# Kernel tuning notes

Measured on AMD Instinct MI355X. Metric: run time of the kernel, lower is better.

## Reference

```python
import jax, jax.numpy as jnp
import numpy as np
import math

B, T, Z, H, DOF = 256, 200, 64, 256, 12
NUM_LINKS = 13
POS_DIM = (NUM_LINKS + 1) * 3  # 42
TIME_BANDS = 6
TIME_DIM = 2 * TIME_BANDS + 1  # 13
ACTION_SCALE = 0.25
TRACK_ALPHA = 1.0
SIGMA_MIN, SIGMA_MAX = 0.05, 0.5


def setup_inputs() -> dict:
    key = jax.random.key(0)
    ks = iter(jax.random.split(key, 32))
    rn = lambda shape, s=0.1: jax.random.normal(next(ks), shape, jnp.float32) * s
    inp = {
        'z': jax.random.normal(next(ks), (B, Z), jnp.float32),
        'W_hz': rn((H, Z)), 'b_hz': rn((H,)),
        'W_cz': rn((H, Z)), 'b_cz': rn((H,)),
        'Wih': rn((4 * H, DOF + Z + TIME_DIM)), 'Whh': rn((4 * H, H)),
        'bih': rn((4 * H,)), 'bhh': rn((4 * H,)),
        'Wp1': rn((H, H)), 'bp1': rn((H,)),
        'Wp2': rn((DOF, H)), 'bp2': rn((DOF,)),
        'Wo1': rn((H, H)), 'bo1': rn((H,)),
        'Wo2': rn((3, H)), 'bo2': rn((3,)),
        'Wv': rn((POS_DIM, H)), 'bv': rn((POS_DIM,)),
        'Wfk': rn((NUM_LINKS * 3, DOF)), 'bfk': rn((NUM_LINKS * 3,)),
        'pos_mean': jax.random.normal(next(ks), (NUM_LINKS + 1, 3), jnp.float32),
        'pos_std': 0.5 + jax.random.uniform(next(ks), (NUM_LINKS + 1, 3), jnp.float32),
        'joint_lower': -jnp.ones((DOF,), jnp.float32),
        'joint_upper': jnp.ones((DOF,), jnp.float32),
        'default_dof_pos': jnp.zeros((DOF,), jnp.float32),
    }
    return inp


def _time_features():
    t = jnp.linspace(0.0, 1.0, T)
    feats = [t]
    for k in range(TIME_BANDS):
        f = 2.0 ** k
        feats.append(jnp.sin(2 * math.pi * f * t))
        feats.append(jnp.cos(2 * math.pi * f * t))
    return jnp.stack(feats, axis=-1)  # [T, TIME_DIM]


def reference(z, W_hz, b_hz, W_cz, b_cz, Wih, Whh, bih, bhh,
              Wp1, bp1, Wp2, bp2, Wo1, bo1, Wo2, bo2, Wv, bv, Wfk, bfk,
              pos_mean, pos_std, joint_lower, joint_upper, default_dof_pos):
    joint_range = (joint_upper - joint_lower) / 2.0
    joint_mean = (joint_upper + joint_lower) / 2.0
    time_feats = _time_features()  # [T, TIME_DIM]

    h0 = z @ W_hz.T + b_hz  # [B,H]
    c0 = z @ W_cz.T + b_cz
    prev0 = jnp.broadcast_to(default_dof_pos, (B, DOF))

    def step(carry, tf):
        h, c, prev = carry
        prev_norm = (prev - joint_mean) / joint_range
        x = jnp.concatenate([prev_norm, z, jnp.broadcast_to(tf, (B, TIME_DIM))], axis=-1)
        g = x @ Wih.T + bih + h @ Whh.T + bhh  # [B,4H]
        i, f, gg, o = jnp.split(g, 4, axis=-1)
        c_new = jax.nn.sigmoid(f) * c + jax.nn.sigmoid(i) * jnp.tanh(gg)
        h_new = jax.nn.sigmoid(o) * jnp.tanh(c_new)
        action = jnp.tanh(jax.nn.relu(h_new @ Wp1.T + bp1) @ Wp2.T + bp2)
        target = action * ACTION_SCALE + default_dof_pos
        cur = prev + TRACK_ALPHA * (target - prev)
        clamped = jnp.clip(cur, joint_lower, joint_upper)
        cur_in = cur + jax.lax.stop_gradient(clamped - cur)  # straight-through clamp
        obj = jax.nn.relu(h_new @ Wo1.T + bo1) @ Wo2.T + bo2
        return (h_new, c_new, jax.lax.stop_gradient(cur_in)), (h_new, action, cur, obj)

    _, (H_seq, actions, joints, objs) = jax.lax.scan(step, (h0, c0, prev0), time_feats)
    # [T,B,*] -> [B,T,*]
    H_seq = jnp.swapaxes(H_seq, 0, 1)
    actions_seq = jnp.swapaxes(actions, 0, 1)
    joint_traj = jnp.swapaxes(joints, 0, 1)
    object_traj = jnp.swapaxes(objs, 0, 1)

    agent_traj = joint_traj @ Wfk.T + bfk  # FK: [B,T,39]
    combined = jnp.concatenate([agent_traj, object_traj], axis=-1)  # [B,T,42]
    combined_rs = combined.reshape(B, T, NUM_LINKS + 1, 3)
    graph_x_mu = ((combined_rs - pos_mean) / pos_std).reshape(B, T, POS_DIM)

    sigma = SIGMA_MIN + (SIGMA_MAX - SIGMA_MIN) * jax.nn.sigmoid(H_seq @ Wv.T + bv)
    log_sigma_pos = jnp.log(sigma)
    return (graph_x_mu, joint_traj, actions_seq, log_sigma_pos)
```

## Files before the change

kernel.cpp:

```cpp
#include <hip/hip_runtime.h>
#include <math.h>

#define B_ 256
#define T_ 200
#define H_ 256
#define DOF_ 12

typedef __bf16 bf16;
typedef __bf16 bf16x8 __attribute__((ext_vector_type(8)));
typedef float f32x4 __attribute__((ext_vector_type(4)));
typedef unsigned long long u64;

#define XK 288
#define XPAD 296
#define P1PAD 264

#define PI_D 3.14159265358979323846

#define OFF_TF     0u
#define OFF_TCONP  10400u
#define OFF_ZCP    829600u
#define OFF_H0     1878176u
#define OFF_C0     2140320u
#define OFF_WCOMB  2402464u
#define OFF_WP1    2992288u
#define OFF_WP2    3123360u
#define OFF_WO1    3131552u
#define OFF_WO2    3262624u
#define OFF_WV     3270816u
#define OFF_HX     3295392u
#define OFF_HSEQ   3819680u

__device__ __forceinline__ float sigf(float x) { return 1.f / (1.f + __expf(-x)); }
__device__ __forceinline__ float tanh_f(float x) {
  float a = fabsf(x);
  float e = __expf(-2.f * a);
  float t = (1.f - e) * __builtin_amdgcn_rcpf(1.f + e);
  return x < 0.f ? -t : t;
}

#define LBAR() asm volatile("s_waitcnt lgkmcnt(0)\n\ts_barrier" ::: "memory")

__global__ void k_tfeat(float* tf) {
  int i = blockIdx.x * blockDim.x + threadIdx.x;
  if (i >= T_ * 13) return;
  int t = i / 13, j = i % 13;
  float tv = (float)t / 199.f;
  float v;
  if (j == 0) v = tv;
  else {
    int k = (j - 1) >> 1;
    float f = (float)(1 << k);
    double arg = 2.0 * PI_D * (double)f * (double)tv;
    v = (j & 1) ? (float)sin(arg) : (float)cos(arg);
  }
  tf[i] = v;
}

__global__ void k_prep(const float* __restrict__ tf, const float* __restrict__ Wih,
                       const float* __restrict__ z,
                       const float* __restrict__ bih, const float* __restrict__ bhh,
                       const float* __restrict__ Whz, const float* __restrict__ bhz,
                       const float* __restrict__ Wcz, const float* __restrict__ bcz,
                       float* tconp, float* zcp, float* h0, float* c0) {
  int i = blockIdx.x * blockDim.x + threadIdx.x;
  if (i < 204800) {
    int g = i & 3, u = (i >> 2) & 255, t = i >> 10;
    int n = g * 256 + u;
    float s = 0.f;
    #pragma unroll
    for (int j = 0; j < 13; ++j) s += tf[t * 13 + j] * Wih[n * 89 + 76 + j];
    tconp[i] = s;
    return;
  }
  i -= 204800;
  if (i < 262144) {
    int r = i & 3, g = (i >> 2) & 3, tid = (i >> 4) & 255, bid = i >> 12;
    int quarter = bid >> 4, grp = bid & 15;
    int wv = tid >> 6, ln = tid & 63, lr = ln & 15, lq = (ln >> 4) & 3;
    int b = grp * 16 + lq * 4 + r;
    int n = g * 256 + 64 * quarter + 16 * wv + lr;
    float s = bih[n] + bhh[n];
    for (int k = 0; k < 64; ++k) s += z[b * 64 + k] * Wih[n * 89 + 12 + k];
    zcp[i] = s;
    return;
  }
  i -= 262144;
  if (i < 65536) {
    int b = i / 256, u = i % 256;
    float s = bhz[u];
    for (int k = 0; k < 64; ++k) s += z[b * 64 + k] * Whz[u * 64 + k];
    h0[i] = s;
    return;
  }
  i -= 65536;
  if (i < 65536) {
    int b = i / 256, u = i % 256;
    float s = bcz[u];
    for (int k = 0; k < 64; ++k) s += z[b * 64 + k] * Wcz[u * 64 + k];
    c0[i] = s;
  }
}

__global__ void k_cast(const float* __restrict__ Whh, const float* __restrict__ Wih,
                       const float* __restrict__ Wp1, const float* __restrict__ Wp2,
                       const float* __restrict__ Wo1, const float* __restrict__ Wo2,
                       const float* __restrict__ Wv,
                       bf16* Wcomb, bf16* Wp1b, bf16* Wp2b, bf16* Wo1b,
                       bf16* Wo2b, bf16* Wvb) {
  int i = blockIdx.x * blockDim.x + threadIdx.x;
  if (i < 294912) {
    int n = i / XK, k = i % XK;
    float v = (k < 256) ? Whh[n * 256 + k]
            : ((k < 268) ? Wih[n * 89 + (k - 256)] : 0.f);
    Wcomb[i] = (bf16)v;
    return;
  }
  i -= 294912;
  if (i < 65536) { Wp1b[i] = (bf16)Wp1[i]; return; }
  i -= 65536;
  if (i < 4096) { int r = i / 256; Wp2b[i] = (bf16)((r < 12) ? Wp2[i] : 0.f); return; }
  i -= 4096;
  if (i < 65536) { Wo1b[i] = (bf16)Wo1[i]; return; }
  i -= 65536;
  if (i < 4096) { int r = i / 256; Wo2b[i] = (bf16)((r < 3) ? Wo2[i] : 0.f); return; }
  i -= 4096;
  if (i < 12288) { int r = i / 256; Wvb[i] = (bf16)((r < 42) ? Wv[i] : 0.f); }
}

__global__ __launch_bounds__(256, 1) void k_recur(
    const float* __restrict__ zcp, const float* __restrict__ tconp,
    const float* __restrict__ h0, const float* __restrict__ c0,
    const bf16* __restrict__ Wcomb, const bf16* __restrict__ Wp1b,
    const bf16* __restrict__ Wp2b,
    const float* __restrict__ bp1, const float* __restrict__ bp2,
    const float* __restrict__ jlo, const float* __restrict__ jhi,
    const float* __restrict__ ddp,
    u64* hxt,
    bf16* __restrict__ Hseq, float* __restrict__ outJ, float* __restrict__ outA) {
  __shared__ bf16 xbuf[16][XPAD];
  __shared__ bf16 w1[272][P1PAD];
  __shared__ bf16 p1buf[16][P1PAD];
  const int tid = threadIdx.x;
  const int wv = tid >> 6, ln = tid & 63, lr = ln & 15, lq = ln >> 4;
  const int bid = blockIdx.x;
  const int quarter = bid >> 4, grp = bid & 15;
  const int b0 = grp * 16;
  const int u_gl = 64 * quarter + 16 * wv + lr;

  for (int i = tid; i < 272 * 32; i += 256) {
    int r = i >> 5, c8 = (i & 31) * 8;
    bf16x8 v = (r < 256)
      ? *reinterpret_cast<const bf16x8*>(&Wp1b[r * 256 + c8])
      : *reinterpret_cast<const bf16x8*>(&Wp2b[(r - 256) * 256 + c8]);
    *reinterpret_cast<bf16x8*>(&w1[r][c8]) = v;
  }
  for (int i = tid; i < 16 * XPAD; i += 256) {
    int r = i / XPAD, c = i % XPAD;
    float v = 0.f;
    if (c < 256) v = h0[(b0 + r) * 256 + c];
    else if (c < 268) {
      int d = c - 256;
      float lo = jlo[d], hi = jhi[d];
      v = (ddp[d] - 0.5f * (hi + lo)) / (0.5f * (hi - lo));
    }
    xbuf[r][c] = (bf16)v;
  }

  f32x4 wc[4][9];
  #pragma unroll
  for (int g = 0; g < 4; ++g)
    #pragma unroll
    for (int kt = 0; kt < 9; ++kt)
      wc[g][kt] = *reinterpret_cast<const f32x4*>(
          &Wcomb[(size_t)(g * 256 + u_gl) * XK + kt * 32 + lq * 8]);
  #pragma unroll
  for (int kt = 0; kt < 9; ++kt)
    asm volatile("" : "+a"(wc[0][kt]), "+a"(wc[1][kt]),
                      "+a"(wc[2][kt]), "+a"(wc[3][kt]));

  float c_reg[4];
  #pragma unroll
  for (int r = 0; r < 4; ++r) c_reg[r] = c0[(b0 + lq * 4 + r) * 256 + u_gl];
  const int zc_i = (bid * 256 + tid) * 16;
  int tc_i = u_gl * 4;
  int hs_i = ((b0 + lq * 4) * T_) * 256 + u_gl;
  const int pw_i = (grp * 8 + quarter) * 512 + (16 * wv + lr) * 8 + lq * 2;
  const int ru = tid >> 2, rlq = tid & 3;
  const int rrow0 = rlq * 4;
  const int q1 = (quarter + 1) & 3, q2 = (quarter + 2) & 3, q3 = (quarter + 3) & 3;
  const int pr1 = (grp * 8 + q1) * 512 + ru * 8 + rlq * 2;
  const int pr2 = (grp * 8 + q2) * 512 + ru * 8 + rlq * 2;
  const int pr3 = (grp * 8 + q3) * 512 + ru * 8 + rlq * 2;

  float bp1r[4];
  #pragma unroll
  for (int jn = 0; jn < 4; ++jn) bp1r[jn] = bp1[64 * wv + 16 * jn + lr];
  float bp2r = 0.f, ddr = 0.f, lor = -1.f, hir = 1.f;
  if (lr < 12) { bp2r = bp2[lr]; ddr = ddp[lr]; lor = jlo[lr]; hir = jhi[lr]; }
  const float jmr = 0.5f * (hir + lor), jrr = 0.5f * (hir - lor);

  __syncthreads();
  bool dead = false;

  for (int t = 0; t < T_; ++t) {
    f32x4 zc[4], tcv;
    #pragma unroll
    for (int g = 0; g < 4; ++g)
      zc[g] = *reinterpret_cast<const f32x4*>(zcp + zc_i + g * 4);
    tcv = *reinterpret_cast<const f32x4*>(tconp + tc_i);
    tc_i += 1024;

    f32x4 ac[4];
    #pragma unroll
    for (int g = 0; g < 4; ++g) ac[g] = (f32x4){0.f, 0.f, 0.f, 0.f};
    #pragma unroll
    for (int kt = 0; kt < 9; ++kt) {
      bf16x8 a = *reinterpret_cast<const bf16x8*>(&xbuf[lr][kt * 32 + lq * 8]);
      asm volatile("" : "+a"(wc[0][kt]), "+a"(wc[1][kt]),
                        "+a"(wc[2][kt]), "+a"(wc[3][kt]));
      #pragma unroll
      for (int g = 0; g < 4; ++g)
        ac[g] = __builtin_amdgcn_mfma_f32_16x16x32_bf16(
            a, __builtin_bit_cast(bf16x8, wc[g][kt]), ac[g], 0, 0, 0);
    }
    #pragma unroll
    for (int g = 0; g < 4; ++g) ac[g] += zc[g] + tcv[g];
    LBAR();

    const unsigned int want = t + 1;
    bf16 hb[4];
    unsigned short s4[4];
    #pragma unroll
    for (int r = 0; r < 4; ++r) {
      float cn = sigf(ac[1][r]) * c_reg[r] + sigf(ac[0][r]) * tanh_f(ac[2][r]);
      float hn = sigf(ac[3][r]) * tanh_f(cn);
      c_reg[r] = cn;
      bf16 h = (bf16)hn;
      hb[r] = h;
      s4[r] = __builtin_bit_cast(unsigned short, h);
    }
    {
      u64 q0 = ((u64)want << 32) | (u64)s4[0] | ((u64)s4[1] << 16);
      u64 qq1 = ((u64)want << 32) | (u64)s4[2] | ((u64)s4[3] << 16);
      int pwi = pw_i + (t & 1) * 2048;
      __hip_atomic_store(hxt + pwi, q0, __ATOMIC_RELAXED, __HIP_MEMORY_SCOPE_AGENT);
      __hip_atomic_store(hxt + pwi + 1, qq1, __ATOMIC_RELAXED, __HIP_MEMORY_SCOPE_AGENT);
    }
    #pragma unroll
    for (int r = 0; r < 4; ++r) {
      xbuf[lq * 4 + r][u_gl] = hb[r];
      Hseq[hs_i + r * (T_ * 256)] = hb[r];
    }
    hs_i += 256;

    u64 pa0, pa1, pb0, pb1, pc0, pc1;
    {
      const int so = (t & 1) * 2048;
      int guard = 1 << 16;
      for (;;) {
        pa0 = __hip_atomic_load(hxt + pr1 + so, __ATOMIC_RELAXED, __HIP_MEMORY_SCOPE_AGENT);
        pa1 = __hip_atomic_load(hxt + pr1 + so + 1, __ATOMIC_RELAXED, __HIP_MEMORY_SCOPE_AGENT);
        pb0 = __hip_atomic_load(hxt + pr2 + so, __ATOMIC_RELAXED, __HIP_MEMORY_SCOPE_AGENT);
        pb1 = __hip_atomic_load(hxt + pr2 + so + 1, __ATOMIC_RELAXED, __HIP_MEMORY_SCOPE_AGENT);
        pc0 = __hip_atomic_load(hxt + pr3 + so, __ATOMIC_RELAXED, __HIP_MEMORY_SCOPE_AGENT);
        pc1 = __hip_atomic_load(hxt + pr3 + so + 1, __ATOMIC_RELAXED, __HIP_MEMORY_SCOPE_AGENT);
        int ok = ((unsigned)(pa0 >> 32) == want) & ((unsigned)(pa1 >> 32) == want) &
                 ((unsigned)(pb0 >> 32) == want) & ((unsigned)(pb1 >> 32) == want) &
                 ((unsigned)(pc0 >> 32) == want) & ((unsigned)(pc1 >> 32) == want);
        if (__all(ok)) break;
        if (dead || --guard == 0) { dead = true; break; }
      }
    }
    {
      int col1 = 64 * q1 + ru, col2 = 64 * q2 + ru, col3 = 64 * q3 + ru;
      xbuf[rrow0 + 0][col1] = __builtin_bit_cast(bf16, (unsigned short)(pa0));
      xbuf[rrow0 + 1][col1] = __builtin_bit_cast(bf16, (unsigned short)(pa0 >> 16));
      xbuf[rrow0 + 2][col1] = __builtin_bit_cast(bf16, (unsigned short)(pa1));
      xbuf[rrow0 + 3][col1] = __builtin_bit_cast(bf16, (unsigned short)(pa1 >> 16));
      xbuf[rrow0 + 0][col2] = __builtin_bit_cast(bf16, (unsigned short)(pb0));
      xbuf[rrow0 + 1][col2] = __builtin_bit_cast(bf16, (unsigned short)(pb0 >> 16));
      xbuf[rrow0 + 2][col2] = __builtin_bit_cast(bf16, (unsigned short)(pb1));
      xbuf[rrow0 + 3][col2] = __builtin_bit_cast(bf16, (unsigned short)(pb1 >> 16));
      xbuf[rrow0 + 0][col3] = __builtin_bit_cast(bf16, (unsigned short)(pc0));
      xbuf[rrow0 + 1][col3] = __builtin_bit_cast(bf16, (unsigned short)(pc0 >> 16));
      xbuf[rrow0 + 2][col3] = __builtin_bit_cast(bf16, (unsigned short)(pc1));
      xbuf[rrow0 + 3][col3] = __builtin_bit_cast(bf16, (unsigned short)(pc1 >> 16));
    }
    LBAR();

    {
      f32x4 pa[4];
      #pragma unroll
      for (int jn = 0; jn < 4; ++jn)
        pa[jn] = (f32x4){bp1r[jn], bp1r[jn], bp1r[jn], bp1r[jn]};
      #pragma unroll
      for (int kt = 0; kt < 8; ++kt) {
        bf16x8 av = *reinterpret_cast<const bf16x8*>(&xbuf[lr][kt * 32 + lq * 8]);
        #pragma unroll
        for (int jn = 0; jn < 4; ++jn) {
          bf16x8 bv = *reinterpret_cast<const bf16x8*>(
              &w1[64 * wv + 16 * jn + lr][kt * 32 + lq * 8]);
          pa[jn] = __builtin_amdgcn_mfma_f32_16x16x32_bf16(av, bv, pa[jn], 0, 0, 0);
        }
      }
      #pragma unroll
      for (int jn = 0; jn < 4; ++jn)
        #pragma unroll
        for (int r = 0; r < 4; ++r)
          p1buf[lq * 4 + r][64 * wv + 16 * jn + lr] = (bf16)fmaxf(pa[jn][r], 0.f);
    }
    LBAR();

    if (wv == 0) {
      f32x4 acc = {0.f, 0.f, 0.f, 0.f};
      #pragma unroll
      for (int kt = 0; kt < 8; ++kt) {
        bf16x8 ap = *reinterpret_cast<const bf16x8*>(&p1buf[lr][kt * 32 + lq * 8]);
        bf16x8 w2 = *reinterpret_cast<const bf16x8*>(&w1[256 + lr][kt * 32 + lq * 8]);
        acc = __builtin_amdgcn_mfma_f32_16x16x32_bf16(ap, w2, acc, 0, 0, 0);
      }
      if (lr < 12) {
        #pragma unroll
        for (int r = 0; r < 4; ++r) {
          int b = lq * 4 + r;
          float act = tanh_f(acc[r] + bp2r);
          float curp = act * 0.25f + ddr;
          float cl = fminf(fmaxf(curp, lor), hir);
          if (quarter == 0) {
            size_t o = ((size_t)(b0 + b) * T_ + t) * 12 + lr;
            outA[o] = act;
            outJ[o] = curp;
          }
          xbuf[b][256 + lr] = (bf16)((cl - jmr) / jrr);
        }
      }
    }
    LBAR();
  }
}

__global__ __launch_bounds__(256) void k_post(
    const bf16* __restrict__ Hseq, const bf16* __restrict__ Wo1b,
    const bf16* __restrict__ Wo2b, const bf16* __restrict__ Wvb,
    const float* __restrict__ bo1, const float* __restrict__ bo2,
    const float* __restrict__ bv,
    const float* __restrict__ Wfk, const float* __restrict__ bfk,
    const float* __restrict__ pm, const float* __restrict__ ps,
    const float* __restrict__ joints, float* __restrict__ out0,
    float* __restrict__ out3) {
  __shared__ bf16 u1buf[16][P1PAD];
  __shared__ float objbuf[16][3];
  __shared__ float jbuf[16][12];
  const int tid = threadIdx.x;
  const int wv = tid >> 6;
  const int ln = tid & 63;
  const int lr = ln & 15;
  const int lq = ln >> 4;

  bf16x8 wo1f[4][8];
  float bo1r[4];
  #pragma unroll
  for (int jn = 0; jn < 4; ++jn) {
    int n0 = wv * 64 + jn * 16;
    bo1r[jn] = bo1[n0 + lr];
    #pragma unroll
    for (int kt = 0; kt < 8; ++kt)
      wo1f[jn][kt] = *reinterpret_cast<const bf16x8*>(
          &Wo1b[(size_t)(n0 + lr) * 256 + kt * 32 + lq * 8]);
  }
  const int col = (wv - 1) * 16 + lr;
  bf16x8 wvf[8];
  float bvr = 0.f;
  if (wv >= 1) {
    #pragma unroll
    for (int kt = 0; kt < 8; ++kt)
      wvf[kt] = *reinterpret_cast<const bf16x8*>(
          &Wvb[(size_t)col * 256 + kt * 32 + lq * 8]);
    bvr = (col < 42) ? bv[col] : 0.f;
  }
  bf16x8 wo2f[8];
  if (wv == 0) {
    #pragma unroll
    for (int kt = 0; kt < 8; ++kt)
      wo2f[kt] = *reinterpret_cast<const bf16x8*>(
          &Wo2b[(size_t)lr * 256 + kt * 32 + lq * 8]);
  }

  for (int it = 0; it < 10; ++it) {
    int tt = blockIdx.x * 10 + it;
    size_t r0 = (size_t)tt * 16;
    bf16x8 ah[8];
    #pragma unroll
    for (int kt = 0; kt < 8; ++kt)
      ah[kt] = *reinterpret_cast<const bf16x8*>(&Hseq[(r0 + lr) * 256 + kt * 32 + lq * 8]);
    #pragma unroll
    for (int jn = 0; jn < 4; ++jn) {
      int n0 = wv * 64 + jn * 16;
      float bb = bo1r[jn];
      f32x4 acc = {bb, bb, bb, bb};
      #pragma unroll
      for (int kt = 0; kt < 8; ++kt)
        acc = __builtin_amdgcn_mfma_f32_16x16x32_bf16(ah[kt], wo1f[jn][kt], acc, 0, 0, 0);
      #pragma unroll
      for (int r = 0; r < 4; ++r)
        u1buf[lq * 4 + r][n0 + lr] = (bf16)fmaxf(acc[r], 0.f);
    }
    if (wv >= 1) {
      f32x4 acc = {bvr, bvr, bvr, bvr};
      #pragma unroll
      for (int kt = 0; kt < 8; ++kt)
        acc = __builtin_amdgcn_mfma_f32_16x16x32_bf16(ah[kt], wvf[kt], acc, 0, 0, 0);
      if (col < 42) {
        #pragma unroll
        for (int r = 0; r < 4; ++r) {
          float s = 0.05f + 0.45f * sigf(acc[r]);
          out3[(r0 + lq * 4 + r) * 42 + col] = __logf(s);
        }
      }
    }
    if (tid < 192) {
      int rr = tid / 12, d = tid % 12;
      jbuf[rr][d] = joints[(r0 + rr) * 12 + d];
    }
    __syncthreads();
    if (wv == 0) {
      bf16x8 ap[8];
      #pragma unroll
      for (int kt = 0; kt < 8; ++kt)
        ap[kt] = *reinterpret_cast<const bf16x8*>(&u1buf[lr][kt * 32 + lq * 8]);
      f32x4 acc = {0.f, 0.f, 0.f, 0.f};
      #pragma unroll
      for (int kt = 0; kt < 8; ++kt)
        acc = __builtin_amdgcn_mfma_f32_16x16x32_bf16(ap[kt], wo2f[kt], acc, 0, 0, 0);
      if (lr < 3) {
        #pragma unroll
        for (int r = 0; r < 4; ++r)
          objbuf[lq * 4 + r][lr] = acc[r] + bo2[lr];
      }
    }
    __syncthreads();
    for (int e = tid; e < 16 * 42; e += 256) {
      int rr = e / 42, pd = e % 42;
      float v;
      if (pd < 39) {
        float s = bfk[pd];
        #pragma unroll
        for (int d = 0; d < 12; ++d) s += jbuf[rr][d] * Wfk[pd * 12 + d];
        v = s;
      } else v = objbuf[rr][pd - 39];
      out0[(r0 + rr) * 42 + pd] = (v - pm[pd]) / ps[pd];
    }
    __syncthreads();
  }
}

extern "C" void kernel_launch(void* const* d_in, const int* in_sizes, int n_in,
                              void* d_out, int out_size, void* d_ws, size_t ws_size,
                              hipStream_t stream) {
  const float* z   = (const float*)d_in[0];
  const float* Whz = (const float*)d_in[1];
  const float* bhz = (const float*)d_in[2];
  const float* Wcz = (const float*)d_in[3];
  const float* bcz = (const float*)d_in[4];
  const float* Wih = (const float*)d_in[5];
  const float* Whh = (const float*)d_in[6];
  const float* bih = (const float*)d_in[7];
  const float* bhh = (const float*)d_in[8];
  const float* Wp1 = (const float*)d_in[9];
  const float* bp1 = (const float*)d_in[10];
  const float* Wp2 = (const float*)d_in[11];
  const float* bp2 = (const float*)d_in[12];
  const float* Wo1 = (const float*)d_in[13];
  const float* bo1 = (const float*)d_in[14];
  const float* Wo2 = (const float*)d_in[15];
  const float* bo2 = (const float*)d_in[16];
  const float* Wv  = (const float*)d_in[17];
  const float* bv  = (const float*)d_in[18];
  const float* Wfk = (const float*)d_in[19];
  const float* bfk = (const float*)d_in[20];
  const float* pm  = (const float*)d_in[21];
  const float* ps  = (const float*)d_in[22];
  const float* jlo = (const float*)d_in[23];
  const float* jhi = (const float*)d_in[24];
  const float* ddp = (const float*)d_in[25];

  char* ws = (char*)d_ws;
  float* tf    = (float*)(ws + OFF_TF);
  float* tconp = (float*)(ws + OFF_TCONP);
  float* zcp   = (float*)(ws + OFF_ZCP);
  float* h0    = (float*)(ws + OFF_H0);
  float* c0    = (float*)(ws + OFF_C0);
  bf16* Wcomb  = (bf16*)(ws + OFF_WCOMB);
  bf16* Wp1b   = (bf16*)(ws + OFF_WP1);
  bf16* Wp2b   = (bf16*)(ws + OFF_WP2);
  bf16* Wo1b   = (bf16*)(ws + OFF_WO1);
  bf16* Wo2b   = (bf16*)(ws + OFF_WO2);
  bf16* Wvb    = (bf16*)(ws + OFF_WV);
  u64* hxt     = (u64*)(ws + OFF_HX);
  bf16* Hseq   = (bf16*)(ws + OFF_HSEQ);

  float* out  = (float*)d_out;
  float* out0 = out;
  float* outJ = out + 2150400;
  float* outA = out + 2764800;
  float* out3 = out + 3379200;

  k_tfeat<<<11, 256, 0, stream>>>(tf);
  k_prep<<<2336, 256, 0, stream>>>(tf, Wih, z, bih, bhh, Whz, bhz, Wcz, bcz,
                                   tconp, zcp, h0, c0);
  k_cast<<<1744, 256, 0, stream>>>(Whh, Wih, Wp1, Wp2, Wo1, Wo2, Wv,
                                   Wcomb, Wp1b, Wp2b, Wo1b, Wo2b, Wvb);
  k_recur<<<64, 256, 0, stream>>>(zcp, tconp, h0, c0, Wcomb, Wp1b, Wp2b,
                                  bp1, bp2, jlo, jhi, ddp, hxt,
                                  Hseq, outJ, outA);
  k_post<<<320, 256, 0, stream>>>(Hseq, Wo1b, Wo2b, Wvb, bo1, bo2, bv,
                                  Wfk, bfk, pm, ps, outJ, out0, out3);
}
```

Measured before the change: 965.7 us.

## Process two batch groups per block to overlap cross-block polling with compute

Each recurrent block now handles two 16-row batch groups, A and B, halving the grid from 64 to 32 blocks. After computing both groups' LSTM gates, the block polls for group A's remote hidden state and runs A's policy heads while B's neighbour data is still arriving, hiding part of the inter-block wait. The Wp1 weights move from shared memory into AGPR registers, freeing LDS for the second x buffer. The cost is more register pressure and twice the serial work per block each step.

```diff
diff --git a/kernel.cpp b/kernel.cpp
--- a/kernel.cpp
+++ b/kernel.cpp
@@ -138,33 +138,41 @@
     const float* __restrict__ ddp,
     u64* hxt,
     bf16* __restrict__ Hseq, float* __restrict__ outJ, float* __restrict__ outA) {
-  __shared__ bf16 xbuf[16][XPAD];
-  __shared__ bf16 w1[272][P1PAD];
+  __shared__ bf16 xbufA[16][XPAD];
+  __shared__ bf16 xbufB[16][XPAD];
   __shared__ bf16 p1buf[16][P1PAD];
+  __shared__ bf16 w2[16][P1PAD];
   const int tid = threadIdx.x;
   const int wv = tid >> 6, ln = tid & 63, lr = ln & 15, lq = ln >> 4;
   const int bid = blockIdx.x;
-  const int quarter = bid >> 4, grp = bid & 15;
-  const int b0 = grp * 16;
+  const int quarter = bid >> 3, j = bid & 7;
+  const int gA = 2 * j, gB = 2 * j + 1;
+  const int b0A = gA * 16, b0B = gB * 16;
   const int u_gl = 64 * quarter + 16 * wv + lr;
 
-  for (int i = tid; i < 272 * 32; i += 256) {
+  for (int i = tid; i < 16 * 32; i += 256) {
     int r = i >> 5, c8 = (i & 31) * 8;
-    bf16x8 v = (r < 256)
-      ? *reinterpret_cast<const bf16x8*>(&Wp1b[r * 256 + c8])
-      : *reinterpret_cast<const bf16x8*>(&Wp2b[(r - 256) * 256 + c8]);
-    *reinterpret_cast<bf16x8*>(&w1[r][c8]) = v;
+    *reinterpret_cast<bf16x8*>(&w2[r][c8]) =
+        *reinterpret_cast<const bf16x8*>(&Wp2b[r * 256 + c8]);
   }
   for (int i = tid; i < 16 * XPAD; i += 256) {
     int r = i / XPAD, c = i % XPAD;
-    float v = 0.f;
-    if (c < 256) v = h0[(b0 + r) * 256 + c];
-    else if (c < 268) {
+    float vA = 0.f;
+    if (c < 256) vA = 0.f;
+    if (c < 256) {
+      xbufA[r][c] = (bf16)h0[(b0A + r) * 256 + c];
+      xbufB[r][c] = (bf16)h0[(b0B + r) * 256 + c];
+    } else if (c < 268) {
       int d = c - 256;
       float lo = jlo[d], hi = jhi[d];
-      v = (ddp[d] - 0.5f * (hi + lo)) / (0.5f * (hi - lo));
+      bf16 pv = (bf16)((ddp[d] - 0.5f * (hi + lo)) / (0.5f * (hi - lo)));
+      xbufA[r][c] = pv;
+      xbufB[r][c] = pv;
+    } else {
+      xbufA[r][c] = (bf16)0.f;
+      xbufB[r][c] = (bf16)0.f;
     }
-    xbuf[r][c] = (bf16)v;
+    (void)vA;
   }
 
   f32x4 wc[4][9];
@@ -174,24 +182,45 @@
     for (int kt = 0; kt < 9; ++kt)
       wc[g][kt] = *reinterpret_cast<const f32x4*>(
           &Wcomb[(size_t)(g * 256 + u_gl) * XK + kt * 32 + lq * 8]);
+  f32x4 wp[4][8];
+  #pragma unroll
+  for (int jn = 0; jn < 4; ++jn)
+    #pragma unroll
+    for (int kt = 0; kt < 8; ++kt)
+      wp[jn][kt] = *reinterpret_cast<const f32x4*>(
+          &Wp1b[(size_t)(64 * wv + 16 * jn + lr) * 256 + kt * 32 + lq * 8]);
   #pragma unroll
   for (int kt = 0; kt < 9; ++kt)
     asm volatile("" : "+a"(wc[0][kt]), "+a"(wc[1][kt]),
                       "+a"(wc[2][kt]), "+a"(wc[3][kt]));
-
-  float c_reg[4];
-  #pragma unroll
-  for (int r = 0; r < 4; ++r) c_reg[r] = c0[(b0 + lq * 4 + r) * 256 + u_gl];
-  const int zc_i = (bid * 256 + tid) * 16;
+  #pragma unroll
+  for (int kt = 0; kt < 8; ++kt)
+    asm volatile("" : "+a"(wp[0][kt]), "+a"(wp[1][kt]),
+                      "+a"(wp[2][kt]), "+a"(wp[3][kt]));
+
+  float cA[4], cB[4];
+  #pragma unroll
+  for (int r = 0; r < 4; ++r) {
+    cA[r] = c0[(b0A + lq * 4 + r) * 256 + u_gl];
+    cB[r] = c0[(b0B + lq * 4 + r) * 256 + u_gl];
+  }
+  const int zc_iA = ((quarter * 16 + gA) * 256 + tid) * 16;
+  const int zc_iB = ((quarter * 16 + gB) * 256 + tid) * 16;
   int tc_i = u_gl * 4;
-  int hs_i = ((b0 + lq * 4) * T_) * 256 + u_gl;
-  const int pw_i = (grp * 8 + quarter) * 512 + (16 * wv + lr) * 8 + lq * 2;
+  int hs_iA = ((b0A + lq * 4) * T_) * 256 + u_gl;
+  int hs_iB = ((b0B + lq * 4) * T_) * 256 + u_gl;
+  const int pwA = (gA * 8 + quarter) * 512 + (16 * wv + lr) * 8 + lq * 2;
+  const int pwB = (gB * 8 + quarter) * 512 + (16 * wv + lr) * 8 + lq * 2;
   const int ru = tid >> 2, rlq = tid & 3;
   const int rrow0 = rlq * 4;
   const int q1 = (quarter + 1) & 3, q2 = (quarter + 2) & 3, q3 = (quarter + 3) & 3;
-  const int pr1 = (grp * 8 + q1) * 512 + ru * 8 + rlq * 2;
-  const int pr2 = (grp * 8 + q2) * 512 + ru * 8 + rlq * 2;
-  const int pr3 = (grp * 8 + q3) * 512 + ru * 8 + rlq * 2;
+  const int prA1 = (gA * 8 + q1) * 512 + ru * 8 + rlq * 2;
+  const int prA2 = (gA * 8 + q2) * 512 + ru * 8 + rlq * 2;
+  const int prA3 = (gA * 8 + q3) * 512 + ru * 8 + rlq * 2;
+  const int prB1 = (gB * 8 + q1) * 512 + ru * 8 + rlq * 2;
+  const int prB2 = (gB * 8 + q2) * 512 + ru * 8 + rlq * 2;
+  const int prB3 = (gB * 8 + q3) * 512 + ru * 8 + rlq * 2;
+  const int col1 = 64 * q1 + ru, col2 = 64 * q2 + ru, col3 = 64 * q3 + ru;
 
   float bp1r[4];
   #pragma unroll
@@ -203,141 +232,144 @@
   __syncthreads();
   bool dead = false;
 
+#define GATES(XB, ZCI, CREG, PWI, HSI)                                         \
+  {                                                                            \
+    f32x4 zc_[4], tcv_;                                                        \
+    _Pragma("unroll") for (int g = 0; g < 4; ++g)                              \
+        zc_[g] = *reinterpret_cast<const f32x4*>(zcp + (ZCI) + g * 4);         \
+    tcv_ = *reinterpret_cast<const f32x4*>(tconp + tc_i);                      \
+    f32x4 ac_[4];                                                              \
+    _Pragma("unroll") for (int g = 0; g < 4; ++g)                              \
+        ac_[g] = (f32x4){0.f, 0.f, 0.f, 0.f};                                  \
+    _Pragma("unroll") for (int kt = 0; kt < 9; ++kt) {                         \
+      bf16x8 a_ = *reinterpret_cast<const bf16x8*>(&XB[lr][kt * 32 + lq * 8]); \
+      _Pragma("unroll") for (int g = 0; g < 4; ++g)                            \
+          ac_[g] = __builtin_amdgcn_mfma_f32_16x16x32_bf16(                    \
+              a_, __builtin_bit_cast(bf16x8, wc[g][kt]), ac_[g], 0, 0, 0);     \
+    }                                                                          \
+    _Pragma("unroll") for (int g = 0; g < 4; ++g) ac_[g] += zc_[g] + tcv_[g];  \
+    LBAR();                                                                    \
+    unsigned short s4_[4];                                                     \
+    bf16 hb_[4];                                                               \
+    _Pragma("unroll") for (int r = 0; r < 4; ++r) {                            \
+      float cn_ = sigf(ac_[1][r]) * CREG[r] + sigf(ac_[0][r]) * tanh_f(ac_[2][r]); \
+      float hn_ = sigf(ac_[3][r]) * tanh_f(cn_);                               \
+      CREG[r] = cn_;                                                           \
+      bf16 h_ = (bf16)hn_;                                                     \
+      hb_[r] = h_;                                                             \
+      s4_[r] = __builtin_bit_cast(unsigned short, h_);                         \
+    }                                                                          \
+    {                                                                          \
+      u64 q0_ = ((u64)want << 32) | (u64)s4_[0] | ((u64)s4_[1] << 16);         \
+      u64 q1_ = ((u64)want << 32) | (u64)s4_[2] | ((u64)s4_[3] << 16);         \
+      int pwi_ = (PWI) + (t & 1) * 2048;                                       \
+      __hip_atomic_store(hxt + pwi_, q0_, __ATOMIC_RELAXED, __HIP_MEMORY_SCOPE_AGENT); \
+      __hip_atomic_store(hxt + pwi_ + 1, q1_, __ATOMIC_RELAXED, __HIP_MEMORY_SCOPE_AGENT); \
+    }                                                                          \
+    _Pragma("unroll") for (int r = 0; r < 4; ++r) {                            \
+      XB[lq * 4 + r][u_gl] = hb_[r];                                           \
+      Hseq[(HSI) + r * (T_ * 256)] = hb_[r];                                   \
+    }                                                                          \
+  }
+
+#define POLLSC(XB, PR1, PR2, PR3)                                              \
+  {                                                                            \
+    const int so_ = (t & 1) * 2048;                                            \
+    u64 pa0, pa1, pb0, pb1, pc0, pc1;                                          \
+    int guard_ = 1 << 16;                                                      \
+    for (;;) {                                                                 \
+      pa0 = __hip_atomic_load(hxt + (PR1) + so_, __ATOMIC_RELAXED, __HIP_MEMORY_SCOPE_AGENT); \
+      pa1 = __hip_atomic_load(hxt + (PR1) + so_ + 1, __ATOMIC_RELAXED, __HIP_MEMORY_SCOPE_AGENT); \
+      pb0 = __hip_atomic_load(hxt + (PR2) + so_, __ATOMIC_RELAXED, __HIP_MEMORY_SCOPE_AGENT); \
+      pb1 = __hip_atomic_load(hxt + (PR2) + so_ + 1, __ATOMIC_RELAXED, __HIP_MEMORY_SCOPE_AGENT); \
+      pc0 = __hip_atomic_load(hxt + (PR3) + so_, __ATOMIC_RELAXED, __HIP_MEMORY_SCOPE_AGENT); \
+      pc1 = __hip_atomic_load(hxt + (PR3) + so_ + 1, __ATOMIC_RELAXED, __HIP_MEMORY_SCOPE_AGENT); \
+      int ok_ = ((unsigned)(pa0 >> 32) == want) & ((unsigned)(pa1 >> 32) == want) & \
+                ((unsigned)(pb0 >> 32) == want) & ((unsigned)(pb1 >> 32) == want) & \
+                ((unsigned)(pc0 >> 32) == want) & ((unsigned)(pc1 >> 32) == want); \
+      if (__all(ok_)) break;                                                   \
+      if (dead || --guard_ == 0) { dead = true; break; }                       \
+    }                                                                          \
+    XB[rrow0 + 0][col1] = __builtin_bit_cast(bf16, (unsigned short)(pa0));     \
+    XB[rrow0 + 1][col1] = __builtin_bit_cast(bf16, (unsigned short)(pa0 >> 16)); \
+    XB[rrow0 + 2][col1] = __builtin_bit_cast(bf16, (unsigned short)(pa1));     \
+    XB[rrow0 + 3][col1] = __builtin_bit_cast(bf16, (unsigned short)(pa1 >> 16)); \
+    XB[rrow0 + 0][col2] = __builtin_bit_cast(bf16, (unsigned short)(pb0));     \
+    XB[rrow0 + 1][col2] = __builtin_bit_cast(bf16, (unsigned short)(pb0 >> 16)); \
+    XB[rrow0 + 2][col2] = __builtin_bit_cast(bf16, (unsigned short)(pb1));     \
+    XB[rrow0 + 3][col2] = __builtin_bit_cast(bf16, (unsigned short)(pb1 >> 16)); \
+    XB[rrow0 + 0][col3] = __builtin_bit_cast(bf16, (unsigned short)(pc0));     \
+    XB[rrow0 + 1][col3] = __builtin_bit_cast(bf16, (unsigned short)(pc0 >> 16)); \
+    XB[rrow0 + 2][col3] = __builtin_bit_cast(bf16, (unsigned short)(pc1));     \
+    XB[rrow0 + 3][col3] = __builtin_bit_cast(bf16, (unsigned short)(pc1 >> 16)); \
+  }
+
+#define HEADS(XB, CURQ, B0, HALFSEL)                                           \
+  {                                                                            \
+    f32x4 pa_[4];                                                              \
+    _Pragma("unroll") for (int jn = 0; jn < 4; ++jn)                           \
+        pa_[jn] = (f32x4){bp1r[jn], bp1r[jn], bp1r[jn], bp1r[jn]};             \
+    _Pragma("unroll") for (int kt = 0; kt < 8; ++kt) {                         \
+      bf16x8 av_ = *reinterpret_cast<const bf16x8*>(&XB[lr][kt * 32 + lq * 8]); \
+      _Pragma("unroll") for (int jn = 0; jn < 4; ++jn)                         \
+          pa_[jn] = __builtin_amdgcn_mfma_f32_16x16x32_bf16(                   \
+              av_, __builtin_bit_cast(bf16x8, wp[jn][kt]), pa_[jn], 0, 0, 0);  \
+    }                                                                          \
+    _Pragma("unroll") for (int jn = 0; jn < 4; ++jn)                           \
+        _Pragma("unroll") for (int r = 0; r < 4; ++r)                          \
+            p1buf[lq * 4 + r][64 * wv + 16 * jn + lr] = (bf16)fmaxf(pa_[jn][r], 0.f); \
+    LBAR();                                                                    \
+    if (wv == 0) {                                                             \
+      f32x4 acc_ = {0.f, 0.f, 0.f, 0.f};                                       \
+      _Pragma("unroll") for (int kt = 0; kt < 8; ++kt) {                       \
+        bf16x8 ap_ = *reinterpret_cast<const bf16x8*>(&p1buf[lr][kt * 32 + lq * 8]); \
+        bf16x8 w2_ = *reinterpret_cast<const bf16x8*>(&w2[lr][kt * 32 + lq * 8]); \
+        acc_ = __builtin_amdgcn_mfma_f32_16x16x32_bf16(ap_, w2_, acc_, 0, 0, 0); \
+      }                                                                        \
+      if (lr < 12) {                                                           \
+        _Pragma("unroll") for (int r = 0; r < 4; ++r) {                        \
+          int b_ = lq * 4 + r;                                                 \
+          float act_ = tanh_f(acc_[r] + bp2r);                                 \
+          float curp_ = act_ * 0.25f + ddr;                                    \
+          float cl_ = fminf(fmaxf(curp_, lor), hir);                           \
+          if (quarter == 0) {                                                  \
+            size_t o_ = ((size_t)((B0) + b_) * T_ + t) * 12 + lr;              \
+            outA[o_] = act_;                                                   \
+            outJ[o_] = curp_;                                                  \
+          }                                                                    \
+          XB[b_][256 + lr] = (bf16)((cl_ - jmr) / jrr);                        \
+        }                                                                      \
+      }                                                                        \
+    }                                                                          \
+  }
+
   for (int t = 0; t < T_; ++t) {
-    f32x4 zc[4], tcv;
-    #pragma unroll
-    for (int g = 0; g < 4; ++g)
-      zc[g] = *reinterpret_cast<const f32x4*>(zcp + zc_i + g * 4);
-    tcv = *reinterpret_cast<const f32x4*>(tconp + tc_i);
-    tc_i += 1024;
-
-    f32x4 ac[4];
-    #pragma unroll
-    for (int g = 0; g < 4; ++g) ac[g] = (f32x4){0.f, 0.f, 0.f, 0.f};
-    #pragma unroll
-    for (int kt = 0; kt < 9; ++kt) {
-      bf16x8 a = *reinterpret_cast<const bf16x8*>(&xbuf[lr][kt * 32 + lq * 8]);
+    const unsigned int want = t + 1;
+    #pragma unroll
+    for (int kt = 0; kt < 9; ++kt)
       asm volatile("" : "+a"(wc[0][kt]), "+a"(wc[1][kt]),
                         "+a"(wc[2][kt]), "+a"(wc[3][kt]));
-      #pragma unroll
-      for (int g = 0; g < 4; ++g)
-        ac[g] = __builtin_amdgcn_mfma_f32_16x16x32_bf16(
-            a, __builtin_bit_cast(bf16x8, wc[g][kt]), ac[g], 0, 0, 0);
-    }
-    #pragma unroll
-    for (int g = 0; g < 4; ++g) ac[g] += zc[g] + tcv[g];
+    #pragma unroll
+    for (int kt = 0; kt < 8; ++kt)
+      asm volatile("" : "+a"(wp[0][kt]), "+a"(wp[1][kt]),
+                        "+a"(wp[2][kt]), "+a"(wp[3][kt]));
+
+    GATES(xbufA, zc_iA, cA, pwA, hs_iA)
+    GATES(xbufB, zc_iB, cB, pwB, hs_iB)
+    POLLSC(xbufA, prA1, prA2, prA3)
     LBAR();
-
-    const unsigned int want = t + 1;
-    bf16 hb[4];
-    unsigned short s4[4];
-    #pragma unroll
-    for (int r = 0; r < 4; ++r) {
-      float cn = sigf(ac[1][r]) * c_reg[r] + sigf(ac[0][r]) * tanh_f(ac[2][r]);
-      float hn = sigf(ac[3][r]) * tanh_f(cn);
-      c_reg[r] = cn;
-      bf16 h = (bf16)hn;
-      hb[r] = h;
-      s4[r] = __builtin_bit_cast(unsigned short, h);
-    }
-    {
-      u64 q0 = ((u64)want << 32) | (u64)s4[0] | ((u64)s4[1] << 16);
-      u64 qq1 = ((u64)want << 32) | (u64)s4[2] | ((u64)s4[3] << 16);
-      int pwi = pw_i + (t & 1) * 2048;
-      __hip_atomic_store(hxt + pwi, q0, __ATOMIC_RELAXED, __HIP_MEMORY_SCOPE_AGENT);
-      __hip_atomic_store(hxt + pwi + 1, qq1, __ATOMIC_RELAXED, __HIP_MEMORY_SCOPE_AGENT);
-    }
-    #pragma unroll
-    for (int r = 0; r < 4; ++r) {
-      xbuf[lq * 4 + r][u_gl] = hb[r];
-      Hseq[hs_i + r * (T_ * 256)] = hb[r];
-    }
-    hs_i += 256;
-
-    u64 pa0, pa1, pb0, pb1, pc0, pc1;
-    {
-      const int so = (t & 1) * 2048;
-      int guard = 1 << 16;
-      for (;;) {
-        pa0 = __hip_atomic_load(hxt + pr1 + so, __ATOMIC_RELAXED, __HIP_MEMORY_SCOPE_AGENT);
-        pa1 = __hip_atomic_load(hxt + pr1 + so + 1, __ATOMIC_RELAXED, __HIP_MEMORY_SCOPE_AGENT);
-        pb0 = __hip_atomic_load(hxt + pr2 + so, __ATOMIC_RELAXED, __HIP_MEMORY_SCOPE_AGENT);
-        pb1 = __hip_atomic_load(hxt + pr2 + so + 1, __ATOMIC_RELAXED, __HIP_MEMORY_SCOPE_AGENT);
-        pc0 = __hip_atomic_load(hxt + pr3 + so, __ATOMIC_RELAXED, __HIP_MEMORY_SCOPE_AGENT);
-        pc1 = __hip_atomic_load(hxt + pr3 + so + 1, __ATOMIC_RELAXED, __HIP_MEMORY_SCOPE_AGENT);
-        int ok = ((unsigned)(pa0 >> 32) == want) & ((unsigned)(pa1 >> 32) == want) &
-                 ((unsigned)(pb0 >> 32) == want) & ((unsigned)(pb1 >> 32) == want) &
-                 ((unsigned)(pc0 >> 32) == want) & ((unsigned)(pc1 >> 32) == want);
-        if (__all(ok)) break;
-        if (dead || --guard == 0) { dead = true; break; }
-      }
-    }
-    {
-      int col1 = 64 * q1 + ru, col2 = 64 * q2 + ru, col3 = 64 * q3 + ru;
-      xbuf[rrow0 + 0][col1] = __builtin_bit_cast(bf16, (unsigned short)(pa0));
-      xbuf[rrow0 + 1][col1] = __builtin_bit_cast(bf16, (unsigned short)(pa0 >> 16));
-      xbuf[rrow0 + 2][col1] = __builtin_bit_cast(bf16, (unsigned short)(pa1));
-      xbuf[rrow0 + 3][col1] = __builtin_bit_cast(bf16, (unsigned short)(pa1 >> 16));
-      xbuf[rrow0 + 0][col2] = __builtin_bit_cast(bf16, (unsigned short)(pb0));
-      xbuf[rrow0 + 1][col2] = __builtin_bit_cast(bf16, (unsigned short)(pb0 >> 16));
-      xbuf[rrow0 + 2][col2] = __builtin_bit_cast(bf16, (unsigned short)(pb1));
-      xbuf[rrow0 + 3][col2] = __builtin_bit_cast(bf16, (unsigned short)(pb1 >> 16));
-      xbuf[rrow0 + 0][col3] = __builtin_bit_cast(bf16, (unsigned short)(pc0));
-      xbuf[rrow0 + 1][col3] = __builtin_bit_cast(bf16, (unsigned short)(pc0 >> 16));
-      xbuf[rrow0 + 2][col3] = __builtin_bit_cast(bf16, (unsigned short)(pc1));
-      xbuf[rrow0 + 3][col3] = __builtin_bit_cast(bf16, (unsigned short)(pc1 >> 16));
-    }
+    HEADS(xbufA, quarter, b0A, 0)
+    POLLSC(xbufB, prB1, prB2, prB3)
     LBAR();
-
-    {
-      f32x4 pa[4];
-      #pragma unroll
-      for (int jn = 0; jn < 4; ++jn)
-        pa[jn] = (f32x4){bp1r[jn], bp1r[jn], bp1r[jn], bp1r[jn]};
-      #pragma unroll
-      for (int kt = 0; kt < 8; ++kt) {
-        bf16x8 av = *reinterpret_cast<const bf16x8*>(&xbuf[lr][kt * 32 + lq * 8]);
-        #pragma unroll
-        for (int jn = 0; jn < 4; ++jn) {
-          bf16x8 bv = *reinterpret_cast<const bf16x8*>(
-              &w1[64 * wv + 16 * jn + lr][kt * 32 + lq * 8]);
-          pa[jn] = __builtin_amdgcn_mfma_f32_16x16x32_bf16(av, bv, pa[jn], 0, 0, 0);
-        }
-      }
-      #pragma unroll
-      for (int jn = 0; jn < 4; ++jn)
-        #pragma unroll
-        for (int r = 0; r < 4; ++r)
-          p1buf[lq * 4 + r][64 * wv + 16 * jn + lr] = (bf16)fmaxf(pa[jn][r], 0.f);
-    }
+    HEADS(xbufB, quarter, b0B, 1)
     LBAR();
-
-    if (wv == 0) {
-      f32x4 acc = {0.f, 0.f, 0.f, 0.f};
-      #pragma unroll
-      for (int kt = 0; kt < 8; ++kt) {
-        bf16x8 ap = *reinterpret_cast<const bf16x8*>(&p1buf[lr][kt * 32 + lq * 8]);
-        bf16x8 w2 = *reinterpret_cast<const bf16x8*>(&w1[256 + lr][kt * 32 + lq * 8]);
-        acc = __builtin_amdgcn_mfma_f32_16x16x32_bf16(ap, w2, acc, 0, 0, 0);
-      }
-      if (lr < 12) {
-        #pragma unroll
-        for (int r = 0; r < 4; ++r) {
-          int b = lq * 4 + r;
-          float act = tanh_f(acc[r] + bp2r);
-          float curp = act * 0.25f + ddr;
-          float cl = fminf(fmaxf(curp, lor), hir);
-          if (quarter == 0) {
-            size_t o = ((size_t)(b0 + b) * T_ + t) * 12 + lr;
-            outA[o] = act;
-            outJ[o] = curp;
-          }
-          xbuf[b][256 + lr] = (bf16)((cl - jmr) / jrr);
-        }
-      }
-    }
-    LBAR();
-  }
+    tc_i += 1024;
+    hs_iA += 256;
+    hs_iB += 256;
+  }
+#undef GATES
+#undef POLLSC
+#undef HEADS
 }
 
 __global__ __launch_bounds__(256) void k_post(
@@ -511,7 +543,7 @@
                                    tconp, zcp, h0, c0);
   k_cast<<<1744, 256, 0, stream>>>(Whh, Wih, Wp1, Wp2, Wo1, Wo2, Wv,
                                    Wcomb, Wp1b, Wp2b, Wo1b, Wo2b, Wvb);
-  k_recur<<<64, 256, 0, stream>>>(zcp, tconp, h0, c0, Wcomb, Wp1b, Wp2b,
+  k_recur<<<32, 256, 0, stream>>>(zcp, tconp, h0, c0, Wcomb, Wp1b, Wp2b,
                                   bp1, bp2, jlo, jhi, ddp, hxt,
                                   Hseq, outJ, outA);
   k_post<<<320, 256, 0, stream>>>(Hseq, Wo1b, Wo2b, Wvb, bo1, bo2, bv,
```

Measured after the change: 2.048 ms. 112% more time.
